# Kernel tuning notes

Hardware: AMD Instinct MI355X
Metric: run time of the kernel (lower is better)

Reference implementation:

```python
import jax, jax.numpy as jnp
import numpy as np
from functools import partial

CHUNK = 32


def _phi(x):
    return jax.nn.elu(x) + 1.0


def _decay_scan(x, log_d, init):
    """Inclusive causal prefix scan out[t] = d*out[t-1] + x[t].
    x: [B,H,T,D], log_d: [H] (log of per-head decay), init: [B,H,D].
    Chunk-and-chain closed form: within a chunk of size C,
      out[c] = d^c * cumsum(x[s] / d^s) + d^(c+1) * init.
    lax.scan iterates over T/C chunks. Returns (out [B,H,T,D], last [B,H,D])."""
    B, H, T, D = x.shape
    C = min(CHUNK, T)
    assert T % C == 0
    Nc = T // C
    c_idx = jnp.arange(C, dtype=x.dtype)
    lp = log_d[None, :, None, None] * c_idx[None, None, :, None]      # [1,H,C,1]
    p = jnp.exp(lp)
    inv_p = jnp.exp(-lp)
    init_p = jnp.exp(log_d[None, :, None, None] * (c_idx + 1.0)[None, None, :, None])

    xc = x.reshape(B, H, Nc, C, D).transpose(2, 0, 1, 3, 4)           # [Nc,B,H,C,D]

    def step(state, chunk):
        cs = jnp.cumsum(chunk * inv_p, axis=2)                        # [B,H,C,D]
        out = cs * p + state[:, :, None, :] * init_p
        return out[:, :, -1, :], out

    last, outs = jax.lax.scan(step, init, xc)
    out = outs.transpose(1, 2, 0, 3, 4).reshape(B, H, T, D)
    return out, last


def setup_inputs() -> dict:
    key = jax.random.key(0)
    k1, k2, k3, k4, k5 = jax.random.split(key, 5)
    B, T, HID, H = 4, 4096, 1024, 16
    logit = lambda p: float(np.log(p / (1.0 - p)))
    return {
        "x": jax.random.normal(k1, (B, T, HID), dtype=jnp.float32),
        "w_qkv": jax.random.normal(k2, (HID, 3 * HID), dtype=jnp.float32) * 0.02,
        "w_out": jax.random.normal(k3, (2 * HID, HID), dtype=jnp.float32) * 0.02,
        "alpha": jnp.full((H,), logit(0.7), dtype=jnp.float32)
                 + 0.01 * jax.random.normal(k4, (H,), dtype=jnp.float32),
        "beta": jnp.full((H,), logit(0.97), dtype=jnp.float32)
                + 0.01 * jax.random.normal(k5, (H,), dtype=jnp.float32),
    }


def reference(x, w_qkv, w_out, alpha, beta):
    B, T, HID = x.shape
    H = alpha.shape[0]
    D = HID // H
    qkv = x @ w_qkv                                                   # [B,T,3*HID]
    q, k, v = jnp.split(qkv, 3, axis=-1)
    to_bhtd = lambda t: t.reshape(B, T, H, D).transpose(0, 2, 1, 3)
    q = _phi(to_bhtd(q))
    k = _phi(to_bhtd(k))
    v = to_bhtd(v)
    kv = k * v

    log_a = jnp.log(jnp.clip(jax.nn.sigmoid(alpha), 1e-8, None))      # [H]
    log_b = jnp.log(jnp.clip(jax.nn.sigmoid(beta), 1e-8, None))

    z = jnp.zeros((B, H, D), dtype=x.dtype)
    run_kv_f, kv_f1 = _decay_scan(kv, log_a, z)
    run_ks_f, ks_f1 = _decay_scan(k, log_a, z)
    run_kv_s, kv_s1 = _decay_scan(kv, log_b, z)
    run_ks_s, ks_s1 = _decay_scan(k, log_b, z)

    eps = 1e-6
    den_f = jnp.clip(jnp.sum(q * run_ks_f, axis=-1, keepdims=True), eps, None)
    den_s = jnp.clip(jnp.sum(q * run_ks_s, axis=-1, keepdims=True), eps, None)
    out_f = (q * run_kv_f / den_f).transpose(0, 2, 1, 3).reshape(B, T, HID)
    out_s = (q * run_kv_s / den_s).transpose(0, 2, 1, 3).reshape(B, T, HID)
    out = jnp.concatenate([out_f, out_s], axis=-1) @ w_out            # [B,T,HID]
    return out, (kv_f1, ks_f1, kv_s1, ks_s1)
```

## Files before the change

kernel.cpp:

```cpp
#include <hip/hip_runtime.h>
#include <hip/hip_bf16.h>
#include <stdint.h>

#define B_   4
#define T_   4096
#define HID_ 1024
#define H_   16
#define D_   64
#define CCH  64
#define NC_  (T_ / CCH)

typedef __attribute__((ext_vector_type(8))) short short8;
typedef __attribute__((ext_vector_type(4))) float f32x4;

__device__ __forceinline__ float phi_(float x) { return x > 0.f ? x + 1.f : __expf(x); }
__device__ __forceinline__ float sigm_(float x) { return 1.f / (1.f + expf(-x)); }

#define BAR() __builtin_amdgcn_s_barrier()
#define PRIO1() __builtin_amdgcn_s_setprio(1)
#define PRIO0() __builtin_amdgcn_s_setprio(0)
#define SCHED0() __builtin_amdgcn_sched_barrier(0)
#define WAITVM0()   { asm volatile("s_waitcnt vmcnt(0)" ::: "memory"); SCHED0(); }
#define WAITVM8()   { asm volatile("s_waitcnt vmcnt(8)" ::: "memory"); SCHED0(); }
#define WAITLGKM0() { asm volatile("s_waitcnt lgkmcnt(0)" ::: "memory"); SCHED0(); }

__global__ __launch_bounds__(256) void k_cast_bf16(const float* __restrict__ in,
                                                   __hip_bfloat16* __restrict__ out, int n) {
  int i = (blockIdx.x * 256 + threadIdx.x) * 4;
  if (i >= n) return;
  float4 f = *(const float4*)(in + i);
  out[i + 0] = __float2bfloat16(f.x);
  out[i + 1] = __float2bfloat16(f.y);
  out[i + 2] = __float2bfloat16(f.z);
  out[i + 3] = __float2bfloat16(f.w);
}

__global__ __launch_bounds__(256) void k_transpose_cast(const float* __restrict__ in,
                                                        __hip_bfloat16* __restrict__ out,
                                                        int R, int C) {
  __shared__ float tile[32][33];
  int c0 = blockIdx.x * 32, r0 = blockIdx.y * 32;
  int tx = threadIdx.x, ty = threadIdx.y;
#pragma unroll
  for (int i = 0; i < 32; i += 8)
    tile[ty + i][tx] = in[(size_t)(r0 + ty + i) * C + c0 + tx];
  __syncthreads();
#pragma unroll
  for (int i = 0; i < 32; i += 8)
    out[(size_t)(c0 + ty + i) * R + r0 + tx] = __float2bfloat16(tile[tx][ty + i]);
}

__device__ __forceinline__ void gload_lds16(const __hip_bfloat16* g, const __hip_bfloat16* lds) {
  __builtin_amdgcn_global_load_lds(
      (const __attribute__((address_space(1))) uint32_t*)(uintptr_t)g,
      (__attribute__((address_space(3))) uint32_t*)(uintptr_t)lds, 16, 0, 0);
}

template <typename OutT>
__global__ __launch_bounds__(512, 2) void k_gemm256(const __hip_bfloat16* __restrict__ A,
                                                    const __hip_bfloat16* __restrict__ BT,
                                                    OutT* __restrict__ C,
                                                    int M, int N, int K) {
  __shared__ __hip_bfloat16 lds[65536];
  const int tid = threadIdx.x, lane = tid & 63, wid = tid >> 6;
  const int wm = wid >> 2, wn = wid & 3;
  const int r16 = lane & 15, k8 = ((lane >> 4) & 3) * 8;

  const int bid = blockIdx.x;
  const int MT = M >> 8;
  const int Rb = MT >> 3;
  const int x = bid & 7, ii = bid >> 3;
  const int rt = x * Rb + (ii % Rb), ct = ii / Rb;
  const int bm = rt << 8, bn = ct << 8;

  const int sRow = wid * 8 + (lane >> 3);
  const int sCol = ((lane & 7) * 8) ^ ((lane >> 3) << 3);
  const __hip_bfloat16* gA = A  + (size_t)(bm + sRow) * K + sCol;
  const __hip_bfloat16* gB = BT + (size_t)(bn + sRow) * K + sCol;

  auto stageA2 = [&](int buf, int kt, int half) {
#pragma unroll
    for (int cc = 0; cc < 2; ++cc)
      gload_lds16(gA + (size_t)(half * 2 + cc) * 64 * K + kt,
                  &lds[buf * 32768 + (half * 2 + cc) * 4096 + wid * 512]);
  };
  auto stageB2 = [&](int buf, int kt, int half) {
#pragma unroll
    for (int cc = 0; cc < 2; ++cc)
      gload_lds16(gB + (size_t)(half * 2 + cc) * 64 * K + kt,
                  &lds[buf * 32768 + 16384 + (half * 2 + cc) * 4096 + wid * 512]);
  };
  auto ldA = [&](int buf, int m, int kk) -> short8 {
    int row = wm * 128 + m * 16 + r16;
    int col = (kk * 32 + k8) ^ ((row & 7) << 3);
    return *(const short8*)&lds[buf * 32768 + (row << 6) + col];
  };
  auto ldB = [&](int buf, int n, int kk) -> short8 {
    int row = wn * 64 + n * 16 + r16;
    int col = (kk * 32 + k8) ^ ((row & 7) << 3);
    return *(const short8*)&lds[buf * 32768 + 16384 + (row << 6) + col];
  };

  f32x4 acc[8][4] = {};
  const int NT = K >> 6;

  stageA2(0, 0, 0);  stageA2(0, 0, 1);  stageB2(0, 0, 0);  stageB2(0, 0, 1);
  stageA2(1, 64, 0); stageA2(1, 64, 1); stageB2(1, 64, 0); stageB2(1, 64, 1);
  WAITVM8(); BAR();

  short8 a[8][2], bfr[4][2];
  for (int t = 0; t < NT; ++t) {
    const int cb = t & 1;
    const bool pf = (t + 2 < NT);
    const int kt2 = (t + 2) << 6;
#pragma unroll
    for (int m = 0; m < 8; ++m) { a[m][0] = ldA(cb, m, 0); a[m][1] = ldA(cb, m, 1); }
#pragma unroll
    for (int n = 0; n < 4; ++n) { bfr[n][0] = ldB(cb, n, 0); bfr[n][1] = ldB(cb, n, 1); }
    WAITLGKM0();
    BAR();
    PRIO1();
#pragma unroll
    for (int m = 0; m < 2; ++m)
#pragma unroll
      for (int n = 0; n < 4; ++n) {
        acc[m][n] = __builtin_amdgcn_mfma_f32_16x16x32_bf16(a[m][0], bfr[n][0], acc[m][n], 0, 0, 0);
        acc[m][n] = __builtin_amdgcn_mfma_f32_16x16x32_bf16(a[m][1], bfr[n][1], acc[m][n], 0, 0, 0);
      }
    PRIO0();
    if (pf) stageA2(cb, kt2, 0);
    PRIO1();
#pragma unroll
    for (int m = 2; m < 4; ++m)
#pragma unroll
      for (int n = 0; n < 4; ++n) {
        acc[m][n] = __builtin_amdgcn_mfma_f32_16x16x32_bf16(a[m][0], bfr[n][0], acc[m][n], 0, 0, 0);
        acc[m][n] = __builtin_amdgcn_mfma_f32_16x16x32_bf16(a[m][1], bfr[n][1], acc[m][n], 0, 0, 0);
      }
    PRIO0();
    if (pf) stageA2(cb, kt2, 1);
    PRIO1();
#pragma unroll
    for (int m = 4; m < 6; ++m)
#pragma unroll
      for (int n = 0; n < 4; ++n) {
        acc[m][n] = __builtin_amdgcn_mfma_f32_16x16x32_bf16(a[m][0], bfr[n][0], acc[m][n], 0, 0, 0);
        acc[m][n] = __builtin_amdgcn_mfma_f32_16x16x32_bf16(a[m][1], bfr[n][1], acc[m][n], 0, 0, 0);
      }
    PRIO0();
    if (pf) stageB2(cb, kt2, 0);
    PRIO1();
#pragma unroll
    for (int m = 6; m < 8; ++m)
#pragma unroll
      for (int n = 0; n < 4; ++n) {
        acc[m][n] = __builtin_amdgcn_mfma_f32_16x16x32_bf16(a[m][0], bfr[n][0], acc[m][n], 0, 0, 0);
        acc[m][n] = __builtin_amdgcn_mfma_f32_16x16x32_bf16(a[m][1], bfr[n][1], acc[m][n], 0, 0, 0);
      }
    PRIO0();
    if (pf)              { stageB2(cb, kt2, 1); WAITVM8(); }
    else if (t + 1 < NT) { WAITVM0(); }
    BAR();
  }

#pragma unroll
  for (int m = 0; m < 8; ++m)
#pragma unroll
    for (int n = 0; n < 4; ++n)
#pragma unroll
      for (int j = 0; j < 4; ++j) {
        int row = bm + wm * 128 + m * 16 + ((lane >> 4) << 2) + j;
        int col = bn + wn * 64 + n * 16 + r16;
        if constexpr (sizeof(OutT) == 4)
          C[(size_t)row * N + col] = acc[m][n][j];
        else
          C[(size_t)row * N + col] = __float2bfloat16(acc[m][n][j]);
      }
}

__global__ __launch_bounds__(64) void k_scan1(const __hip_bfloat16* __restrict__ qkv,
                                              const float* __restrict__ alpha,
                                              const float* __restrict__ beta,
                                              float* __restrict__ chunkL) {
  int blk = blockIdx.x;
  int c = blk & (NC_ - 1), h = (blk >> 6) & (H_ - 1), b = blk >> 10;
  int d = threadIdx.x;
  float da = fmaxf(sigm_(alpha[h]), 1e-8f);
  float db = fmaxf(sigm_(beta[h]), 1e-8f);
  const __hip_bfloat16* base = qkv + (size_t)(b * T_ + c * CCH) * (3 * HID_) + h * D_ + d;
  float l0 = 0.f, l1 = 0.f, l2 = 0.f, l3 = 0.f;
#pragma unroll 4
  for (int t = 0; t < CCH; ++t) {
    float k = phi_(__bfloat162float(base[HID_]));
    float v = __bfloat162float(base[2 * HID_]);
    float kv = k * v;
    l0 = da * l0 + kv; l1 = da * l1 + k;
    l2 = db * l2 + kv; l3 = db * l3 + k;
    base += 3 * HID_;
  }
  size_t S = (size_t)B_ * H_ * NC_ * D_;
  size_t idx = (((size_t)(b * H_ + h)) * NC_ + c) * D_ + d;
  chunkL[idx] = l0; chunkL[S + idx] = l1; chunkL[2 * S + idx] = l2; chunkL[3 * S + idx] = l3;
}

__global__ __launch_bounds__(256) void k_scan2(const float* __restrict__ chunkL,
                                               const float* __restrict__ alpha,
                                               const float* __restrict__ beta,
                                               float* __restrict__ carry,
                                               float* __restrict__ out_tail) {
  int t = blockIdx.x * 256 + threadIdx.x;
  int d = t & (D_ - 1), h = (t >> 6) & (H_ - 1), b = t >> 10;
  float da = fmaxf(sigm_(alpha[h]), 1e-8f);
  float db = fmaxf(sigm_(beta[h]), 1e-8f);
  float daC = da, dbC = db;
#pragma unroll
  for (int i = 0; i < 6; ++i) { daC *= daC; dbC *= dbC; }
  size_t S = (size_t)B_ * H_ * NC_ * D_;
  size_t base = ((size_t)(b * H_ + h)) * NC_ * D_ + d;
  float s0 = 0.f, s1 = 0.f, s2 = 0.f, s3 = 0.f;
  for (int c = 0; c < NC_; ++c) {
    size_t idx = base + (size_t)c * D_;
    carry[idx] = s0; carry[S + idx] = s1; carry[2 * S + idx] = s2; carry[3 * S + idx] = s3;
    s0 = daC * s0 + chunkL[idx];
    s1 = daC * s1 + chunkL[S + idx];
    s2 = dbC * s2 + chunkL[2 * S + idx];
    s3 = dbC * s3 + chunkL[3 * S + idx];
  }
  int fi = (b * H_ + h) * D_ + d;
  out_tail[fi] = s0;
  out_tail[B_ * H_ * D_ + fi] = s1;
  out_tail[2 * B_ * H_ * D_ + fi] = s2;
  out_tail[3 * B_ * H_ * D_ + fi] = s3;
}

__global__ __launch_bounds__(64) void k_scan3(const __hip_bfloat16* __restrict__ qkv,
                                              const float* __restrict__ carry,
                                              const float* __restrict__ alpha,
                                              const float* __restrict__ beta,
                                              __hip_bfloat16* __restrict__ ocat) {
  int blk = blockIdx.x;
  int c = blk & (NC_ - 1), h = (blk >> 6) & (H_ - 1), b = blk >> 10;
  int d = threadIdx.x;
  float da = fmaxf(sigm_(alpha[h]), 1e-8f);
  float db = fmaxf(sigm_(beta[h]), 1e-8f);
  size_t S = (size_t)B_ * H_ * NC_ * D_;
  size_t cidx = (((size_t)(b * H_ + h)) * NC_ + c) * D_ + d;
  float s0 = carry[cidx], s1 = carry[S + cidx], s2 = carry[2 * S + cidx], s3 = carry[3 * S + cidx];
  const __hip_bfloat16* base = qkv + (size_t)(b * T_ + c * CCH) * (3 * HID_) + h * D_ + d;
  __hip_bfloat16* ob = ocat + (size_t)(b * T_ + c * CCH) * (2 * HID_) + h * D_ + d;
#pragma unroll 4
  for (int t = 0; t < CCH; ++t) {
    float q = phi_(__bfloat162float(base[0]));
    float k = phi_(__bfloat162float(base[HID_]));
    float v = __bfloat162float(base[2 * HID_]);
    float kv = k * v;
    s0 = da * s0 + kv; s1 = da * s1 + k;
    s2 = db * s2 + kv; s3 = db * s3 + k;
    float pf = q * s1, ps = q * s3;
#pragma unroll
    for (int off = 32; off >= 1; off >>= 1) {
      pf += __shfl_xor(pf, off);
      ps += __shfl_xor(ps, off);
    }
    pf = fmaxf(pf, 1e-6f);
    ps = fmaxf(ps, 1e-6f);
    ob[0]    = __float2bfloat16(q * s0 / pf);
    ob[HID_] = __float2bfloat16(q * s2 / ps);
    base += 3 * HID_;
    ob += 2 * HID_;
  }
}

extern "C" void kernel_launch(void* const* d_in, const int* in_sizes, int n_in,
                              void* d_out, int out_size, void* d_ws, size_t ws_size,
                              hipStream_t stream) {
  const float* x     = (const float*)d_in[0];
  const float* wqkv  = (const float*)d_in[1];
  const float* wout  = (const float*)d_in[2];
  const float* alpha = (const float*)d_in[3];
  const float* beta  = (const float*)d_in[4];
  float* out = (float*)d_out;

  char* ws = (char*)d_ws;
  __hip_bfloat16* qkv    = (__hip_bfloat16*)(ws);
  char*           reg1   = ws + (size_t)B_ * T_ * 3 * HID_ * 2;
  __hip_bfloat16* ocat   = (__hip_bfloat16*)reg1;
  __hip_bfloat16* xb     = (__hip_bfloat16*)reg1;
  __hip_bfloat16* wqkvT  = (__hip_bfloat16*)(reg1 + (size_t)B_ * T_ * HID_ * 2);
  char*           p2     = reg1 + (size_t)B_ * T_ * 2 * HID_ * 2;
  __hip_bfloat16* woutT  = (__hip_bfloat16*)p2;
  float*          chunkL = (float*)(p2 + (size_t)2 * HID_ * HID_ * 2);
  float*          carry  = (float*)(p2 + (size_t)2 * HID_ * HID_ * 2 + (size_t)4 * B_ * H_ * NC_ * D_ * 4);
  (void)ws_size; (void)in_sizes; (void)n_in; (void)out_size;

  int nx = B_ * T_ * HID_;
  k_cast_bf16<<<nx / 1024, 256, 0, stream>>>(x, xb, nx);
  k_transpose_cast<<<dim3(3 * HID_ / 32, HID_ / 32), dim3(32, 8), 0, stream>>>(wqkv, wqkvT, HID_, 3 * HID_);
  k_transpose_cast<<<dim3(HID_ / 32, 2 * HID_ / 32), dim3(32, 8), 0, stream>>>(wout, woutT, 2 * HID_, HID_);
  k_gemm256<__hip_bfloat16><<<(B_ * T_ / 256) * (3 * HID_ / 256), 512, 0, stream>>>(xb, wqkvT, qkv, B_ * T_, 3 * HID_, HID_);
  k_scan1<<<B_ * H_ * NC_, 64, 0, stream>>>(qkv, alpha, beta, chunkL);
  k_scan2<<<(B_ * H_ * D_) / 256, 256, 0, stream>>>(chunkL, alpha, beta, carry, out + (size_t)B_ * T_ * HID_);
  k_scan3<<<B_ * H_ * NC_, 64, 0, stream>>>(qkv, carry, alpha, beta, ocat);
  k_gemm256<float><<<(B_ * T_ / 256) * (HID_ / 256), 512, 0, stream>>>(ocat, woutT, out, B_ * T_, HID_, 2 * HID_);
}
```

Baseline: 268.6 us.

## Software-pipeline GEMM LDS fragment loads across k-halves with register double buffering

Restructures the GEMM main loop so LDS fragment reads for the second k-half (and the next tile's first k-half) are issued while MFMAs on the already-loaded half run. This uses two register sets instead of loading all fragments and then waiting. Global-to-LDS staging is now issued in one batch after the barrier rather than interleaved between MFMA groups. The aim is to hide LDS read latency behind matrix compute. The cost is an extra barrier per iteration and less overlap of global loads with compute.

```diff
diff --git a/kernel.cpp b/kernel.cpp
--- a/kernel.cpp
+++ b/kernel.cpp
@@ -78,17 +78,13 @@
   const __hip_bfloat16* gA = A  + (size_t)(bm + sRow) * K + sCol;
   const __hip_bfloat16* gB = BT + (size_t)(bn + sRow) * K + sCol;
 
-  auto stageA2 = [&](int buf, int kt, int half) {
-#pragma unroll
-    for (int cc = 0; cc < 2; ++cc)
-      gload_lds16(gA + (size_t)(half * 2 + cc) * 64 * K + kt,
-                  &lds[buf * 32768 + (half * 2 + cc) * 4096 + wid * 512]);
-  };
-  auto stageB2 = [&](int buf, int kt, int half) {
-#pragma unroll
-    for (int cc = 0; cc < 2; ++cc)
-      gload_lds16(gB + (size_t)(half * 2 + cc) * 64 * K + kt,
-                  &lds[buf * 32768 + 16384 + (half * 2 + cc) * 4096 + wid * 512]);
+  auto stage = [&](int buf, int kt) {
+#pragma unroll
+    for (int cc = 0; cc < 4; ++cc)
+      gload_lds16(gA + (size_t)cc * 64 * K + kt, &lds[buf * 32768 + cc * 4096 + wid * 512]);
+#pragma unroll
+    for (int cc = 0; cc < 4; ++cc)
+      gload_lds16(gB + (size_t)cc * 64 * K + kt, &lds[buf * 32768 + 16384 + cc * 4096 + wid * 512]);
   };
   auto ldA = [&](int buf, int m, int kk) -> short8 {
     int row = wm * 128 + m * 16 + r16;
@@ -104,63 +100,49 @@
   f32x4 acc[8][4] = {};
   const int NT = K >> 6;
 
-  stageA2(0, 0, 0);  stageA2(0, 0, 1);  stageB2(0, 0, 0);  stageB2(0, 0, 1);
-  stageA2(1, 64, 0); stageA2(1, 64, 1); stageB2(1, 64, 0); stageB2(1, 64, 1);
+  short8 A0[8], B0[4], A1[8], B1[4];
+
+  stage(0, 0);
+  stage(1, 64);
   WAITVM8(); BAR();
-
-  short8 a[8][2], bfr[4][2];
+#pragma unroll
+  for (int m = 0; m < 8; ++m) A0[m] = ldA(0, m, 0);
+#pragma unroll
+  for (int n = 0; n < 4; ++n) B0[n] = ldB(0, n, 0);
+  SCHED0();
+
   for (int t = 0; t < NT; ++t) {
     const int cb = t & 1;
-    const bool pf = (t + 2 < NT);
-    const int kt2 = (t + 2) << 6;
-#pragma unroll
-    for (int m = 0; m < 8; ++m) { a[m][0] = ldA(cb, m, 0); a[m][1] = ldA(cb, m, 1); }
-#pragma unroll
-    for (int n = 0; n < 4; ++n) { bfr[n][0] = ldB(cb, n, 0); bfr[n][1] = ldB(cb, n, 1); }
+#pragma unroll
+    for (int m = 0; m < 8; ++m) A1[m] = ldA(cb, m, 1);
+#pragma unroll
+    for (int n = 0; n < 4; ++n) B1[n] = ldB(cb, n, 1);
+    SCHED0();
+    PRIO1();
+#pragma unroll
+    for (int m = 0; m < 8; ++m)
+#pragma unroll
+      for (int n = 0; n < 4; ++n)
+        acc[m][n] = __builtin_amdgcn_mfma_f32_16x16x32_bf16(A0[m], B0[n], acc[m][n], 0, 0, 0);
+    PRIO0();
     WAITLGKM0();
     BAR();
+    if (t + 2 < NT)      { stage(cb, (t + 2) << 6); WAITVM8(); BAR(); }
+    else if (t + 1 < NT) { WAITVM0(); BAR(); }
+    if (t + 1 < NT) {
+#pragma unroll
+      for (int m = 0; m < 8; ++m) A0[m] = ldA(cb ^ 1, m, 0);
+#pragma unroll
+      for (int n = 0; n < 4; ++n) B0[n] = ldB(cb ^ 1, n, 0);
+      SCHED0();
+    }
     PRIO1();
 #pragma unroll
-    for (int m = 0; m < 2; ++m)
-#pragma unroll
-      for (int n = 0; n < 4; ++n) {
-        acc[m][n] = __builtin_amdgcn_mfma_f32_16x16x32_bf16(a[m][0], bfr[n][0], acc[m][n], 0, 0, 0);
-        acc[m][n] = __builtin_amdgcn_mfma_f32_16x16x32_bf16(a[m][1], bfr[n][1], acc[m][n], 0, 0, 0);
-      }
+    for (int m = 0; m < 8; ++m)
+#pragma unroll
+      for (int n = 0; n < 4; ++n)
+        acc[m][n] = __builtin_amdgcn_mfma_f32_16x16x32_bf16(A1[m], B1[n], acc[m][n], 0, 0, 0);
     PRIO0();
-    if (pf) stageA2(cb, kt2, 0);
-    PRIO1();
-#pragma unroll
-    for (int m = 2; m < 4; ++m)
-#pragma unroll
-      for (int n = 0; n < 4; ++n) {
-        acc[m][n] = __builtin_amdgcn_mfma_f32_16x16x32_bf16(a[m][0], bfr[n][0], acc[m][n], 0, 0, 0);
-        acc[m][n] = __builtin_amdgcn_mfma_f32_16x16x32_bf16(a[m][1], bfr[n][1], acc[m][n], 0, 0, 0);
-      }
-    PRIO0();
-    if (pf) stageA2(cb, kt2, 1);
-    PRIO1();
-#pragma unroll
-    for (int m = 4; m < 6; ++m)
-#pragma unroll
-      for (int n = 0; n < 4; ++n) {
-        acc[m][n] = __builtin_amdgcn_mfma_f32_16x16x32_bf16(a[m][0], bfr[n][0], acc[m][n], 0, 0, 0);
-        acc[m][n] = __builtin_amdgcn_mfma_f32_16x16x32_bf16(a[m][1], bfr[n][1], acc[m][n], 0, 0, 0);
-      }
-    PRIO0();
-    if (pf) stageB2(cb, kt2, 0);
-    PRIO1();
-#pragma unroll
-    for (int m = 6; m < 8; ++m)
-#pragma unroll
-      for (int n = 0; n < 4; ++n) {
-        acc[m][n] = __builtin_amdgcn_mfma_f32_16x16x32_bf16(a[m][0], bfr[n][0], acc[m][n], 0, 0, 0);
-        acc[m][n] = __builtin_amdgcn_mfma_f32_16x16x32_bf16(a[m][1], bfr[n][1], acc[m][n], 0, 0, 0);
-      }
-    PRIO0();
-    if (pf)              { stageB2(cb, kt2, 1); WAITVM8(); }
-    else if (t + 1 < NT) { WAITVM0(); }
-    BAR();
   }
 
 #pragma unroll
```

After: 263.4 us. Within noise of the previous version (-1.9%).

## Fuse prep casts into one kernel and add split-K-step pipelined GEMM for output projection

Applied to the files above, without the earlier changes.

Three preprocessing launches (x cast and two weight transposes) become one kernel that dispatches on block index, and the x cast now uses wider 8-element vector stores. The output-projection GEMM gets a new variant that stages whole 64-wide K tiles for A and B in a double buffer, then interleaves LDS fragment loads for the second k-half with MFMAs on the first half. The aim is to cut launch overhead and hide LDS latency in the K=2048 GEMM. The QKV GEMM is unchanged apart from its name. The new schedule adds more barriers per K step and holds more fragment registers.

```diff
diff --git a/kernel.cpp b/kernel.cpp
--- a/kernel.cpp
+++ b/kernel.cpp
@@ -24,23 +24,39 @@
 #define WAITVM8()   { asm volatile("s_waitcnt vmcnt(8)" ::: "memory"); SCHED0(); }
 #define WAITLGKM0() { asm volatile("s_waitcnt lgkmcnt(0)" ::: "memory"); SCHED0(); }
 
-__global__ __launch_bounds__(256) void k_cast_bf16(const float* __restrict__ in,
-                                                   __hip_bfloat16* __restrict__ out, int n) {
-  int i = (blockIdx.x * 256 + threadIdx.x) * 4;
-  if (i >= n) return;
-  float4 f = *(const float4*)(in + i);
-  out[i + 0] = __float2bfloat16(f.x);
-  out[i + 1] = __float2bfloat16(f.y);
-  out[i + 2] = __float2bfloat16(f.z);
-  out[i + 3] = __float2bfloat16(f.w);
-}
-
-__global__ __launch_bounds__(256) void k_transpose_cast(const float* __restrict__ in,
-                                                        __hip_bfloat16* __restrict__ out,
-                                                        int R, int C) {
+#define NB_CAST (B_ * T_ * HID_ / 2048)
+#define NB_TQ   ((3 * HID_ / 32) * (HID_ / 32))
+#define NB_TO   ((HID_ / 32) * (2 * HID_ / 32))
+__global__ __launch_bounds__(256) void k_prep(const float* __restrict__ x,
+                                              const float* __restrict__ wqkv,
+                                              const float* __restrict__ wout,
+                                              __hip_bfloat16* __restrict__ xb,
+                                              __hip_bfloat16* __restrict__ wqkvT,
+                                              __hip_bfloat16* __restrict__ woutT) {
+  int bid = blockIdx.x, tid = threadIdx.x;
+  if (bid < NB_CAST) {
+    size_t i = (size_t)bid * 2048 + tid * 8;
+    float4 f0 = *(const float4*)(x + i);
+    float4 f1 = *(const float4*)(x + i + 4);
+    union { short8 v; unsigned short u[8]; } o;
+    o.u[0] = __bfloat16_as_ushort(__float2bfloat16(f0.x));
+    o.u[1] = __bfloat16_as_ushort(__float2bfloat16(f0.y));
+    o.u[2] = __bfloat16_as_ushort(__float2bfloat16(f0.z));
+    o.u[3] = __bfloat16_as_ushort(__float2bfloat16(f0.w));
+    o.u[4] = __bfloat16_as_ushort(__float2bfloat16(f1.x));
+    o.u[5] = __bfloat16_as_ushort(__float2bfloat16(f1.y));
+    o.u[6] = __bfloat16_as_ushort(__float2bfloat16(f1.z));
+    o.u[7] = __bfloat16_as_ushort(__float2bfloat16(f1.w));
+    *(short8*)(xb + i) = o.v;
+    return;
+  }
   __shared__ float tile[32][33];
-  int c0 = blockIdx.x * 32, r0 = blockIdx.y * 32;
-  int tx = threadIdx.x, ty = threadIdx.y;
+  const float* in; __hip_bfloat16* out; int R, C, tb;
+  if (bid < NB_CAST + NB_TQ) { in = wqkv; out = wqkvT; R = HID_; C = 3 * HID_; tb = bid - NB_CAST; }
+  else                       { in = wout; out = woutT; R = 2 * HID_; C = HID_; tb = bid - NB_CAST - NB_TQ; }
+  int nbx = C / 32;
+  int c0 = (tb % nbx) * 32, r0 = (tb / nbx) * 32;
+  int tx = tid & 31, ty = tid >> 5;
 #pragma unroll
   for (int i = 0; i < 32; i += 8)
     tile[ty + i][tx] = in[(size_t)(r0 + ty + i) * C + c0 + tx];
@@ -57,18 +73,17 @@
 }
 
 template <typename OutT>
-__global__ __launch_bounds__(512, 2) void k_gemm256(const __hip_bfloat16* __restrict__ A,
-                                                    const __hip_bfloat16* __restrict__ BT,
-                                                    OutT* __restrict__ C,
-                                                    int M, int N, int K) {
+__global__ __launch_bounds__(512, 2) void k_gemmA(const __hip_bfloat16* __restrict__ A,
+                                                  const __hip_bfloat16* __restrict__ BT,
+                                                  OutT* __restrict__ C,
+                                                  int M, int N, int K) {
   __shared__ __hip_bfloat16 lds[65536];
   const int tid = threadIdx.x, lane = tid & 63, wid = tid >> 6;
   const int wm = wid >> 2, wn = wid & 3;
   const int r16 = lane & 15, k8 = ((lane >> 4) & 3) * 8;
 
   const int bid = blockIdx.x;
-  const int MT = M >> 8;
-  const int Rb = MT >> 3;
+  const int MT = M >> 8, Rb = MT >> 3;
   const int x = bid & 7, ii = bid >> 3;
   const int rt = x * Rb + (ii % Rb), ct = ii / Rb;
   const int bm = rt << 8, bn = ct << 8;
@@ -161,6 +176,108 @@
     if (pf)              { stageB2(cb, kt2, 1); WAITVM8(); }
     else if (t + 1 < NT) { WAITVM0(); }
     BAR();
+  }
+
+#pragma unroll
+  for (int m = 0; m < 8; ++m)
+#pragma unroll
+    for (int n = 0; n < 4; ++n)
+#pragma unroll
+      for (int j = 0; j < 4; ++j) {
+        int row = bm + wm * 128 + m * 16 + ((lane >> 4) << 2) + j;
+        int col = bn + wn * 64 + n * 16 + r16;
+        if constexpr (sizeof(OutT) == 4)
+          C[(size_t)row * N + col] = acc[m][n][j];
+        else
+          C[(size_t)row * N + col] = __float2bfloat16(acc[m][n][j]);
+      }
+}
+
+template <typename OutT>
+__global__ __launch_bounds__(512, 2) void k_gemmB(const __hip_bfloat16* __restrict__ A,
+                                                  const __hip_bfloat16* __restrict__ BT,
+                                                  OutT* __restrict__ C,
+                                                  int M, int N, int K) {
+  __shared__ __hip_bfloat16 lds[65536];
+  const int tid = threadIdx.x, lane = tid & 63, wid = tid >> 6;
+  const int wm = wid >> 2, wn = wid & 3;
+  const int r16 = lane & 15, k8 = ((lane >> 4) & 3) * 8;
+
+  const int bid = blockIdx.x;
+  const int MT = M >> 8, Rb = MT >> 3;
+  const int x = bid & 7, ii = bid >> 3;
+  const int rt = x * Rb + (ii % Rb), ct = ii / Rb;
+  const int bm = rt << 8, bn = ct << 8;
+
+  const int sRow = wid * 8 + (lane >> 3);
+  const int sCol = ((lane & 7) * 8) ^ ((lane >> 3) << 3);
+  const __hip_bfloat16* gA = A  + (size_t)(bm + sRow) * K + sCol;
+  const __hip_bfloat16* gB = BT + (size_t)(bn + sRow) * K + sCol;
+
+  auto stage = [&](int buf, int kt) {
+#pragma unroll
+    for (int cc = 0; cc < 4; ++cc)
+      gload_lds16(gA + (size_t)cc * 64 * K + kt, &lds[buf * 32768 + cc * 4096 + wid * 512]);
+#pragma unroll
+    for (int cc = 0; cc < 4; ++cc)
+      gload_lds16(gB + (size_t)cc * 64 * K + kt, &lds[buf * 32768 + 16384 + cc * 4096 + wid * 512]);
+  };
+  auto ldA = [&](int buf, int m, int kk) -> short8 {
+    int row = wm * 128 + m * 16 + r16;
+    int col = (kk * 32 + k8) ^ ((row & 7) << 3);
+    return *(const short8*)&lds[buf * 32768 + (row << 6) + col];
+  };
+  auto ldB = [&](int buf, int n, int kk) -> short8 {
+    int row = wn * 64 + n * 16 + r16;
+    int col = (kk * 32 + k8) ^ ((row & 7) << 3);
+    return *(const short8*)&lds[buf * 32768 + 16384 + (row << 6) + col];
+  };
+
+  f32x4 acc[8][4] = {};
+  const int NT = K >> 6;
+
+  short8 A0[8], B0[4], A1[8], B1[4];
+  stage(0, 0);
+  stage(1, 64);
+  WAITVM8(); BAR();
+#pragma unroll
+  for (int m = 0; m < 8; ++m) A0[m] = ldA(0, m, 0);
+#pragma unroll
+  for (int n = 0; n < 4; ++n) B0[n] = ldB(0, n, 0);
+  SCHED0();
+
+  for (int t = 0; t < NT; ++t) {
+    const int cb = t & 1;
+#pragma unroll
+    for (int m = 0; m < 8; ++m) A1[m] = ldA(cb, m, 1);
+#pragma unroll
+    for (int n = 0; n < 4; ++n) B1[n] = ldB(cb, n, 1);
+    SCHED0();
+    PRIO1();
+#pragma unroll
+    for (int m = 0; m < 8; ++m)
+#pragma unroll
+      for (int n = 0; n < 4; ++n)
+        acc[m][n] = __builtin_amdgcn_mfma_f32_16x16x32_bf16(A0[m], B0[n], acc[m][n], 0, 0, 0);
+    PRIO0();
+    WAITLGKM0();
+    BAR();
+    if (t + 2 < NT)      { stage(cb, (t + 2) << 6); WAITVM8(); BAR(); }
+    else if (t + 1 < NT) { WAITVM0(); BAR(); }
+    if (t + 1 < NT) {
+#pragma unroll
+      for (int m = 0; m < 8; ++m) A0[m] = ldA(cb ^ 1, m, 0);
+#pragma unroll
+      for (int n = 0; n < 4; ++n) B0[n] = ldB(cb ^ 1, n, 0);
+      SCHED0();
+    }
+    PRIO1();
+#pragma unroll
+    for (int m = 0; m < 8; ++m)
+#pragma unroll
+      for (int n = 0; n < 4; ++n)
+        acc[m][n] = __builtin_amdgcn_mfma_f32_16x16x32_bf16(A1[m], B1[n], acc[m][n], 0, 0, 0);
+    PRIO0();
   }
 
 #pragma unroll
@@ -293,13 +410,12 @@
   float*          carry  = (float*)(p2 + (size_t)2 * HID_ * HID_ * 2 + (size_t)4 * B_ * H_ * NC_ * D_ * 4);
   (void)ws_size; (void)in_sizes; (void)n_in; (void)out_size;
 
-  int nx = B_ * T_ * HID_;
-  k_cast_bf16<<<nx / 1024, 256, 0, stream>>>(x, xb, nx);
-  k_transpose_cast<<<dim3(3 * HID_ / 32, HID_ / 32), dim3(32, 8), 0, stream>>>(wqkv, wqkvT, HID_, 3 * HID_);
-  k_transpose_cast<<<dim3(HID_ / 32, 2 * HID_ / 32), dim3(32, 8), 0, stream>>>(wout, woutT, 2 * HID_, HID_);
-  k_gemm256<__hip_bfloat16><<<(B_ * T_ / 256) * (3 * HID_ / 256), 512, 0, stream>>>(xb, wqkvT, qkv, B_ * T_, 3 * HID_, HID_);
+  k_prep<<<NB_CAST + NB_TQ + NB_TO, 256, 0, stream>>>(x, wqkv, wout, xb, wqkvT, woutT);
+  k_gemmA<__hip_bfloat16><<<(B_ * T_ / 256) * (3 * HID_ / 256), 512, 0, stream>>>(
+      xb, wqkvT, qkv, B_ * T_, 3 * HID_, HID_);
   k_scan1<<<B_ * H_ * NC_, 64, 0, stream>>>(qkv, alpha, beta, chunkL);
   k_scan2<<<(B_ * H_ * D_) / 256, 256, 0, stream>>>(chunkL, alpha, beta, carry, out + (size_t)B_ * T_ * HID_);
   k_scan3<<<B_ * H_ * NC_, 64, 0, stream>>>(qkv, carry, alpha, beta, ocat);
-  k_gemm256<float><<<(B_ * T_ / 256) * (HID_ / 256), 512, 0, stream>>>(ocat, woutT, out, B_ * T_, HID_, 2 * HID_);
-}
+  k_gemmB<float><<<(B_ * T_ / 256) * (HID_ / 256), 512, 0, stream>>>(
+      ocat, woutT, out, B_ * T_, HID_, 2 * HID_);
+}
```

Measured after the change: 258.6 us. 1.04x faster.
